# Kernel optimization log

Hardware: AMD Instinct MI355X
Metric: run time of the kernel (lower is better)

## Reference

```python
import jax, jax.numpy as jnp
import numpy as np

N_HEADS = 8

def setup_inputs() -> dict:
    key = jax.random.key(0)
    ks = jax.random.split(key, 7)
    B, S, D = 4, 2048, 512
    s = 1.0 / np.sqrt(D)
    return {
        "input_Q": jax.random.normal(ks[0], (B, S, D), jnp.float32),
        "input_K": jax.random.normal(ks[1], (B, S, D), jnp.float32),
        "input_V": jax.random.normal(ks[2], (B, S, D), jnp.float32),
        "W_Q": jax.random.normal(ks[3], (D, D), jnp.float32) * s,
        "W_K": jax.random.normal(ks[4], (D, D), jnp.float32) * s,
        "W_V": jax.random.normal(ks[5], (D, D), jnp.float32) * s,
        "W_O": jax.random.normal(ks[6], (D, D), jnp.float32) * s,
    }

def reference(input_Q, input_K, input_V, W_Q, W_K, W_V, W_O):
    B, Sq, D = input_Q.shape
    Sk = input_K.shape[1]
    H = N_HEADS
    d_k = D // H
    # torch nn.Linear(bias=False): y = x @ W.T
    def proj(x, W):
        return (x @ W.T).reshape(B, -1, H, d_k).transpose(0, 2, 1, 3)  # [B,H,S,dk]
    Q = proj(input_Q, W_Q)
    K = proj(input_K, W_K)
    V = proj(input_V, W_V)
    scale = 1.0 / jnp.sqrt(jnp.float32(d_k))
    scores = jnp.einsum("bhqd,bhkd->bhqk", Q, K) * scale  # [B,H,Sq,Sk]
    # TriangularCausalMask: mask strict upper triangle with -inf
    causal = jnp.tril(jnp.ones((Sq, Sk), dtype=bool))
    scores = jnp.where(causal[None, None], scores, -jnp.inf)
    attn = jax.nn.softmax(scores, axis=-1)
    context = jnp.einsum("bhqk,bhkd->bhqd", attn, V)
    context = context.transpose(0, 2, 1, 3).reshape(B, Sq, D)
    return context @ W_O.T
```

## Files before the change

kernel.cpp:

```cpp
#include <hip/hip_runtime.h>
#include <hip/hip_bf16.h>
#include <math.h>

#define B_  4
#define S_  2048
#define D_  512
#define H_  8
#define DK_ 64
#define M_  (B_ * S_)

using bf16   = __bf16;
using bf16x4 = __bf16 __attribute__((ext_vector_type(4)));
using bf16x8 = __bf16 __attribute__((ext_vector_type(8)));
using f32x4  = float __attribute__((ext_vector_type(4)));

#define MFMA16(a, b, c) __builtin_amdgcn_mfma_f32_16x16x32_bf16((a), (b), (c), 0, 0, 0)
#define EXP2(x) exp2f(x)

typedef __attribute__((address_space(3))) void       lds_void;
typedef const __attribute__((address_space(1))) void gbl_void;

__device__ __forceinline__ void async16(const bf16* g, bf16* lds) {
    __builtin_amdgcn_global_load_lds((gbl_void*)g, (lds_void*)lds, 16, 0, 0);
}

__device__ __forceinline__ bf16x8 ldg8(const bf16* p) {
    return *reinterpret_cast<const bf16x8*>(p);
}

__global__ __launch_bounds__(256) void cvt_all(
    const float* __restrict__ x0, const float* __restrict__ x1, const float* __restrict__ x2,
    const float* __restrict__ w0, const float* __restrict__ w1,
    const float* __restrict__ w2, const float* __restrict__ w3,
    bf16* __restrict__ dst)
{
    const size_t i = ((size_t)blockIdx.x * 256 + threadIdx.x) * 8;
    const float* src;
    size_t off;
    if (i < (size_t)3 << 22) {
        const int seg = (int)(i >> 22);
        off = i & (((size_t)1 << 22) - 1);
        src = (seg == 0) ? x0 : (seg == 1) ? x1 : x2;
    } else {
        const size_t j = i - ((size_t)3 << 22);
        const int seg = (int)(j >> 18);
        off = j & (((size_t)1 << 18) - 1);
        src = (seg == 0) ? w0 : (seg == 1) ? w1 : (seg == 2) ? w2 : w3;
    }
    f32x4 a = *reinterpret_cast<const f32x4*>(src + off);
    f32x4 b = *reinterpret_cast<const f32x4*>(src + off + 4);
    bf16x8 r;
    #pragma unroll
    for (int j = 0; j < 4; ++j) { r[j] = (bf16)a[j]; r[j + 4] = (bf16)b[j]; }
    *reinterpret_cast<bf16x8*>(dst + i) = r;
}

template <int MODE>
__global__ __launch_bounds__(256) void gemm_proj(
    const bf16* __restrict__ Xbase, const bf16* __restrict__ Wbase,
    void* __restrict__ OutBase)
{
    const int bx  = blockIdx.x;
    const int xcd = bx & 7;
    const int idx = bx >> 3;
    const int mt  = xcd + 8 * (idx & 7);
    const int nt  = (MODE == 0) ? ((idx >> 3) & 3) : (idx >> 3);
    const int z   = (MODE == 0) ? (idx >> 5) : 3;

    const bf16* X  = Xbase + ((MODE == 0) ? (size_t)z * M_ * D_ : 0);
    const bf16* Wm = Wbase + (size_t)z * D_ * D_;

    const int lane = threadIdx.x & 63;
    const int wave = threadIdx.x >> 6;
    const int lc = lane & 15;
    const int lg = lane >> 4;
    const int ta = (wave >> 1) * 4;
    const int tb = (wave & 1) * 4;
    const int wblk = nt * 128;
    const int xblk = mt * 128;
    const bool swapped = (MODE == 1) || (z < 2);

    __shared__ bf16 As[2][128 * 64];
    __shared__ bf16 Bs[2][128 * 64];

    f32x4 acc[4][4] = {};

    #pragma unroll
    for (int i = 0; i < 4; ++i) {
        const int g   = i * 4 + wave;
        const int row = (g & 7) * 16 + lc;
        const int kc  = (g >> 3) * 4 + lg;
        async16(X  + (size_t)(xblk + row) * D_ + kc * 8, As[0] + (i * 256 + wave * 64) * 8);
        async16(Wm + (size_t)(wblk + row) * D_ + kc * 8, Bs[0] + (i * 256 + wave * 64) * 8);
    }

    for (int j = 0; j < 8; ++j) {
        __syncthreads();
        if (j < 7) {
            const int kn = (j + 1) * 64;
            bf16* ad = As[(j + 1) & 1];
            bf16* bd = Bs[(j + 1) & 1];
            #pragma unroll
            for (int i = 0; i < 4; ++i) {
                const int g   = i * 4 + wave;
                const int row = (g & 7) * 16 + lc;
                const int kc  = (g >> 3) * 4 + lg;
                async16(X  + (size_t)(xblk + row) * D_ + kn + kc * 8,
                        ad + (i * 256 + wave * 64) * 8);
                async16(Wm + (size_t)(wblk + row) * D_ + kn + kc * 8,
                        bd + (i * 256 + wave * 64) * 8);
            }
        }
        const bf16* as = As[j & 1];
        const bf16* bs = Bs[j & 1];

        #pragma unroll
        for (int kk = 0; kk < 2; ++kk) {
            bf16x8 af[4], bfm[4];
            if (swapped) {
                #pragma unroll
                for (int mi = 0; mi < 4; ++mi)
                    af[mi] = ldg8(&bs[(kk * 512 + (ta + mi) * 64 + lane) * 8]);
                #pragma unroll
                for (int ni = 0; ni < 4; ++ni)
                    bfm[ni] = ldg8(&as[(kk * 512 + (tb + ni) * 64 + lane) * 8]);
            } else {
                #pragma unroll
                for (int mi = 0; mi < 4; ++mi)
                    af[mi] = ldg8(&as[(kk * 512 + (ta + mi) * 64 + lane) * 8]);
                #pragma unroll
                for (int ni = 0; ni < 4; ++ni)
                    bfm[ni] = ldg8(&bs[(kk * 512 + (tb + ni) * 64 + lane) * 8]);
            }
            #pragma unroll
            for (int mi = 0; mi < 4; ++mi)
                #pragma unroll
                for (int ni = 0; ni < 4; ++ni)
                    acc[mi][ni] = MFMA16(af[mi], bfm[ni], acc[mi][ni]);
        }
    }

    if (MODE == 1) {
        float* Y = (float*)OutBase;
        #pragma unroll
        for (int mi = 0; mi < 4; ++mi)
            #pragma unroll
            for (int ni = 0; ni < 4; ++ni) {
                const int s = xblk + (tb + ni) * 16 + lc;
                const int d = wblk + (ta + mi) * 16 + lg * 4;
                *reinterpret_cast<f32x4*>(&Y[(size_t)s * D_ + d]) = acc[mi][ni];
            }
    } else if (z < 2) {
        bf16* Y = (bf16*)OutBase + (size_t)z * M_ * D_;
        const float sc = (z == 0) ? 0.125f * 1.4426950408889634f : 1.0f;
        #pragma unroll
        for (int mi = 0; mi < 4; ++mi)
            #pragma unroll
            for (int ni = 0; ni < 4; ++ni) {
                const int s = xblk + (tb + ni) * 16 + lc;
                const int d = wblk + (ta + mi) * 16 + lg * 4;
                bf16x4 v;
                #pragma unroll
                for (int r = 0; r < 4; ++r) v[r] = (bf16)(acc[mi][ni][r] * sc);
                const size_t oidx =
                    ((((size_t)(s >> 11) * H_ + (d >> 6)) * S_
                      + (s & (S_ - 1))) << 6) + (d & 63);
                *reinterpret_cast<bf16x4*>(&Y[oidx]) = v;
            }
    } else {
        bf16* Y = (bf16*)OutBase + (size_t)z * M_ * D_;
        #pragma unroll
        for (int mi = 0; mi < 4; ++mi)
            #pragma unroll
            for (int ni = 0; ni < 4; ++ni) {
                const int s0  = xblk + (ta + mi) * 16 + lg * 4;
                const int col = wblk + (tb + ni) * 16 + lc;
                bf16x4 v;
                #pragma unroll
                for (int r = 0; r < 4; ++r) v[r] = (bf16)acc[mi][ni][r];
                const size_t oidx =
                    ((((size_t)(s0 >> 11)) * H_ + (col >> 6)) << 17)
                    + (size_t)(col & 63) * S_ + (s0 & (S_ - 1));
                *reinterpret_cast<bf16x4*>(&Y[oidx]) = v;
            }
    }
}

__global__ __launch_bounds__(256) void attn(
    const bf16* __restrict__ QKV, bf16* __restrict__ Ctx)
{
    const int bx = blockIdx.x;
    const int bh = (bx & 7) * 4 + ((bx >> 3) & 3);
    const int pi = bx >> 5;
    const int b = bh >> 3, h = bh & 7;
    const size_t plane = (size_t)S_ * DK_;
    const bf16* Q  = QKV + (size_t)bh * plane;
    const bf16* Kp = QKV + (size_t)(B_ * H_) * plane + (size_t)bh * plane;
    const bf16* Vt = QKV + 2 * (size_t)(B_ * H_) * plane + (size_t)bh * plane;

    const int lane = threadIdx.x & 63;
    const int wave = threadIdx.x >> 6;
    const int lc = lane & 15;
    const int lg = lane >> 4;
    const int srow = wave * 16 + lc;
    const int mrow = wave * 16 + lc;

    __shared__ bf16 Ks[2][64 * 64];
    __shared__ bf16 Vs[2][64 * 64];
    __shared__ bf16 Pw[4][128 * 8];

    const int lo = pi;
    const int hi = 31 - pi;

    const int qL = lo * 64 + mrow;
    const int qH = hi * 64 + mrow;
    bf16x8 qfL0 = ldg8(Q + (size_t)qL * DK_ + lg * 8);
    bf16x8 qfL1 = ldg8(Q + (size_t)qL * DK_ + 32 + lg * 8);
    bf16x8 qfH0 = ldg8(Q + (size_t)qH * DK_ + lg * 8);
    bf16x8 qfH1 = ldg8(Q + (size_t)qH * DK_ + 32 + lg * 8);

    f32x4 accL[4] = {}, accH[4] = {};
    float liL = 0.f, liH = 0.f;

    #pragma unroll
    for (int i = 0; i < 2; ++i) {
        const int kc = i * 4 + lg;
        async16(Kp + (size_t)srow * DK_ + kc * 8, Ks[0] + (i * 256 + wave * 64) * 8);
        async16(Vt + (size_t)srow * S_ + kc * 8,  Vs[0] + (i * 256 + wave * 64) * 8);
    }

    for (int j = 0; j <= hi; ++j) {
        __syncthreads();
        if (j < hi) {
            const int kn = (j + 1) * 64;
            bf16* kd = Ks[(j + 1) & 1];
            bf16* vd = Vs[(j + 1) & 1];
            #pragma unroll
            for (int i = 0; i < 2; ++i) {
                const int kc = i * 4 + lg;
                async16(Kp + (size_t)(kn + srow) * DK_ + kc * 8,
                        kd + (i * 256 + wave * 64) * 8);
                async16(Vt + (size_t)srow * S_ + kn + kc * 8,
                        vd + (i * 256 + wave * 64) * 8);
            }
        }
        const bf16* ks = Ks[j & 1];
        const bf16* vs = Vs[j & 1];
        bf16* Pp = &Pw[wave][0];

        bf16x8 kf0[4], kf1[4], vf0[4], vf1[4];
        #pragma unroll
        for (int t = 0; t < 4; ++t) {
            kf0[t] = ldg8(&ks[(t * 64 + lane) * 8]);
            kf1[t] = ldg8(&ks[(256 + t * 64 + lane) * 8]);
            vf0[t] = ldg8(&vs[(t * 64 + lane) * 8]);
            vf1[t] = ldg8(&vs[(256 + t * 64 + lane) * 8]);
        }

        auto step = [&](const bf16x8& qf0, const bf16x8& qf1, bool diag,
                        f32x4* accO, float& li) {
            f32x4 st[4];
            #pragma unroll
            for (int t = 0; t < 4; ++t) {
                f32x4 zz = {};
                zz = MFMA16(kf0[t], qf0, zz);
                st[t] = MFMA16(kf1[t], qf1, zz);
            }
            float rs = 0.f;
            if (diag) {
                #pragma unroll
                for (int t = 0; t < 4; ++t)
                    #pragma unroll
                    for (int r = 0; r < 4; ++r) {
                        const int kl = t * 16 + lg * 4 + r;
                        const float pv = EXP2((kl <= mrow) ? st[t][r] : -1e30f);
                        st[t][r] = pv;
                        rs += pv;
                    }
            } else {
                #pragma unroll
                for (int t = 0; t < 4; ++t)
                    #pragma unroll
                    for (int r = 0; r < 4; ++r) {
                        const float pv = EXP2(st[t][r]);
                        st[t][r] = pv;
                        rs += pv;
                    }
            }
            li += rs;

            #pragma unroll
            for (int t = 0; t < 4; ++t) {
                bf16x4 pv;
                #pragma unroll
                for (int r = 0; r < 4; ++r) pv[r] = (bf16)st[t][r];
                *reinterpret_cast<bf16x4*>(
                    &Pp[((2 * t + (lg >> 1)) * 16 + lc) * 8 + (lg & 1) * 4]) = pv;
            }
            bf16x8 p0 = ldg8(&Pp[lane * 8]);
            bf16x8 p1 = ldg8(&Pp[(64 + lane) * 8]);

            #pragma unroll
            for (int t = 0; t < 4; ++t) {
                accO[t] = MFMA16(vf0[t], p0, accO[t]);
                accO[t] = MFMA16(vf1[t], p1, accO[t]);
            }
        };

        step(qfH0, qfH1, j == hi, accH, liH);
        if (j <= lo) step(qfL0, qfL1, j == lo, accL, liL);
    }

    liL += __shfl_xor(liL, 16); liL += __shfl_xor(liL, 32);
    liH += __shfl_xor(liH, 16); liH += __shfl_xor(liH, 32);
    const float rlL = 1.0f / liL;
    const float rlH = 1.0f / liH;
    #pragma unroll
    for (int t = 0; t < 4; ++t) {
        bf16x4 oL, oH;
        #pragma unroll
        for (int r = 0; r < 4; ++r) {
            oL[r] = (bf16)(accL[t][r] * rlL);
            oH[r] = (bf16)(accH[t][r] * rlH);
        }
        const int d = t * 16 + lg * 4;
        *reinterpret_cast<bf16x4*>(&Ctx[((size_t)b * S_ + qL) * D_ + h * 64 + d]) = oL;
        *reinterpret_cast<bf16x4*>(&Ctx[((size_t)b * S_ + qH) * D_ + h * 64 + d]) = oH;
    }
}

extern "C" void kernel_launch(void* const* d_in, const int* in_sizes, int n_in,
                              void* d_out, int out_size, void* d_ws, size_t ws_size,
                              hipStream_t stream)
{
    float* out = (float*)d_out;

    bf16* Xb  = (bf16*)d_ws;
    bf16* Wb  = Xb + (size_t)3 * M_ * D_;
    bf16* qkv = Wb + (size_t)4 * D_ * D_;
    bf16* ctx = qkv + (size_t)3 * M_ * D_;

    cvt_all<<<6656, 256, 0, stream>>>(
        (const float*)d_in[0], (const float*)d_in[1], (const float*)d_in[2],
        (const float*)d_in[3], (const float*)d_in[4], (const float*)d_in[5],
        (const float*)d_in[6], Xb);

    gemm_proj<0><<<dim3(768), 256, 0, stream>>>(Xb, Wb, qkv);
    attn<<<dim3(512), 256, 0, stream>>>(qkv, ctx);
    gemm_proj<1><<<dim3(256), 256, 0, stream>>>(ctx, Wb, out);
}
```

Before: 196.4 us.

## Store operands in MFMA fragment layout and drop LDS staging in projection GEMMs

Result: faster. 188.4 us (-4.1%).

```diff
diff --git a/kernel.cpp b/kernel.cpp
--- a/kernel.cpp
+++ b/kernel.cpp
@@ -28,6 +28,10 @@
     return *reinterpret_cast<const bf16x8*>(p);
 }
 
+__device__ __forceinline__ size_t fragbase(int g, int k0, int kk, int t) {
+    return ((((size_t)(g * 8 + k0) * 2 + kk) * 4 + t) * 64) * 8;
+}
+
 __global__ __launch_bounds__(256) void cvt_all(
     const float* __restrict__ x0, const float* __restrict__ x1, const float* __restrict__ x2,
     const float* __restrict__ w0, const float* __restrict__ w1,
@@ -36,102 +40,70 @@
 {
     const size_t i = ((size_t)blockIdx.x * 256 + threadIdx.x) * 8;
     const float* src;
-    size_t off;
+    size_t off, dbase;
     if (i < (size_t)3 << 22) {
         const int seg = (int)(i >> 22);
         off = i & (((size_t)1 << 22) - 1);
         src = (seg == 0) ? x0 : (seg == 1) ? x1 : x2;
+        dbase = (size_t)seg << 22;
     } else {
-        const size_t j = i - ((size_t)3 << 22);
-        const int seg = (int)(j >> 18);
-        off = j & (((size_t)1 << 18) - 1);
+        const size_t jj = i - ((size_t)3 << 22);
+        const int seg = (int)(jj >> 18);
+        off = jj & (((size_t)1 << 18) - 1);
         src = (seg == 0) ? w0 : (seg == 1) ? w1 : (seg == 2) ? w2 : w3;
-    }
+        dbase = ((size_t)3 << 22) + ((size_t)seg << 18);
+    }
+    const int row = (int)(off >> 9), col = (int)(off & 511);
+    const int g = row >> 6, t = (row >> 4) & 3, lc = row & 15;
+    const int k0 = col >> 6, kk = (col >> 5) & 1, lg = (col >> 3) & 3;
+    const size_t didx = dbase + fragbase(g, k0, kk, t) + (size_t)(lg * 16 + lc) * 8;
+
     f32x4 a = *reinterpret_cast<const f32x4*>(src + off);
     f32x4 b = *reinterpret_cast<const f32x4*>(src + off + 4);
     bf16x8 r;
     #pragma unroll
     for (int j = 0; j < 4; ++j) { r[j] = (bf16)a[j]; r[j + 4] = (bf16)b[j]; }
-    *reinterpret_cast<bf16x8*>(dst + i) = r;
-}
-
-template <int MODE>
-__global__ __launch_bounds__(256) void gemm_proj(
-    const bf16* __restrict__ Xbase, const bf16* __restrict__ Wbase,
-    void* __restrict__ OutBase)
+    *reinterpret_cast<bf16x8*>(dst + didx) = r;
+}
+
+__global__ __launch_bounds__(256) void gemm_qkv(
+    const bf16* __restrict__ Xf, const bf16* __restrict__ Wf,
+    bf16* __restrict__ qkv)
 {
     const int bx  = blockIdx.x;
     const int xcd = bx & 7;
     const int idx = bx >> 3;
     const int mt  = xcd + 8 * (idx & 7);
-    const int nt  = (MODE == 0) ? ((idx >> 3) & 3) : (idx >> 3);
-    const int z   = (MODE == 0) ? (idx >> 5) : 3;
-
-    const bf16* X  = Xbase + ((MODE == 0) ? (size_t)z * M_ * D_ : 0);
-    const bf16* Wm = Wbase + (size_t)z * D_ * D_;
+    const int rest = idx >> 3;
+    const int nt  = rest & 3;
+    const int z   = rest >> 2;
+
+    const bf16* Xz = Xf + (size_t)z * M_ * D_;
+    const bf16* Wz = Wf + (size_t)z * D_ * D_;
+    const bool vz = (z == 2);
+    const bf16* A  = vz ? Xz : Wz;
+    const bf16* Bm = vz ? Wz : Xz;
 
     const int lane = threadIdx.x & 63;
     const int wave = threadIdx.x >> 6;
     const int lc = lane & 15;
     const int lg = lane >> 4;
-    const int ta = (wave >> 1) * 4;
-    const int tb = (wave & 1) * 4;
-    const int wblk = nt * 128;
-    const int xblk = mt * 128;
-    const bool swapped = (MODE == 1) || (z < 2);
-
-    __shared__ bf16 As[2][128 * 64];
-    __shared__ bf16 Bs[2][128 * 64];
+    const int gA = (vz ? 2 * mt : 2 * nt) + (wave >> 1);
+    const int gB = (vz ? 2 * nt : 2 * mt) + (wave & 1);
 
     f32x4 acc[4][4] = {};
 
     #pragma unroll
-    for (int i = 0; i < 4; ++i) {
-        const int g   = i * 4 + wave;
-        const int row = (g & 7) * 16 + lc;
-        const int kc  = (g >> 3) * 4 + lg;
-        async16(X  + (size_t)(xblk + row) * D_ + kc * 8, As[0] + (i * 256 + wave * 64) * 8);
-        async16(Wm + (size_t)(wblk + row) * D_ + kc * 8, Bs[0] + (i * 256 + wave * 64) * 8);
-    }
-
-    for (int j = 0; j < 8; ++j) {
-        __syncthreads();
-        if (j < 7) {
-            const int kn = (j + 1) * 64;
-            bf16* ad = As[(j + 1) & 1];
-            bf16* bd = Bs[(j + 1) & 1];
-            #pragma unroll
-            for (int i = 0; i < 4; ++i) {
-                const int g   = i * 4 + wave;
-                const int row = (g & 7) * 16 + lc;
-                const int kc  = (g >> 3) * 4 + lg;
-                async16(X  + (size_t)(xblk + row) * D_ + kn + kc * 8,
-                        ad + (i * 256 + wave * 64) * 8);
-                async16(Wm + (size_t)(wblk + row) * D_ + kn + kc * 8,
-                        bd + (i * 256 + wave * 64) * 8);
-            }
-        }
-        const bf16* as = As[j & 1];
-        const bf16* bs = Bs[j & 1];
-
+    for (int k0 = 0; k0 < 8; ++k0) {
         #pragma unroll
         for (int kk = 0; kk < 2; ++kk) {
             bf16x8 af[4], bfm[4];
-            if (swapped) {
-                #pragma unroll
-                for (int mi = 0; mi < 4; ++mi)
-                    af[mi] = ldg8(&bs[(kk * 512 + (ta + mi) * 64 + lane) * 8]);
-                #pragma unroll
-                for (int ni = 0; ni < 4; ++ni)
-                    bfm[ni] = ldg8(&as[(kk * 512 + (tb + ni) * 64 + lane) * 8]);
-            } else {
-                #pragma unroll
-                for (int mi = 0; mi < 4; ++mi)
-                    af[mi] = ldg8(&as[(kk * 512 + (ta + mi) * 64 + lane) * 8]);
-                #pragma unroll
-                for (int ni = 0; ni < 4; ++ni)
-                    bfm[ni] = ldg8(&bs[(kk * 512 + (tb + ni) * 64 + lane) * 8]);
-            }
+            #pragma unroll
+            for (int t = 0; t < 4; ++t)
+                af[t] = ldg8(A + fragbase(gA, k0, kk, t) + (size_t)lane * 8);
+            #pragma unroll
+            for (int t = 0; t < 4; ++t)
+                bfm[t] = ldg8(Bm + fragbase(gB, k0, kk, t) + (size_t)lane * 8);
             #pragma unroll
             for (int mi = 0; mi < 4; ++mi)
                 #pragma unroll
@@ -140,25 +112,15 @@
         }
     }
 
-    if (MODE == 1) {
-        float* Y = (float*)OutBase;
+    if (z < 2) {
+        bf16* Y = qkv + (size_t)z * M_ * D_;
+        const float sc = (z == 0) ? 0.125f * 1.4426950408889634f : 1.0f;
         #pragma unroll
         for (int mi = 0; mi < 4; ++mi)
             #pragma unroll
             for (int ni = 0; ni < 4; ++ni) {
-                const int s = xblk + (tb + ni) * 16 + lc;
-                const int d = wblk + (ta + mi) * 16 + lg * 4;
-                *reinterpret_cast<f32x4*>(&Y[(size_t)s * D_ + d]) = acc[mi][ni];
-            }
-    } else if (z < 2) {
-        bf16* Y = (bf16*)OutBase + (size_t)z * M_ * D_;
-        const float sc = (z == 0) ? 0.125f * 1.4426950408889634f : 1.0f;
-        #pragma unroll
-        for (int mi = 0; mi < 4; ++mi)
-            #pragma unroll
-            for (int ni = 0; ni < 4; ++ni) {
-                const int s = xblk + (tb + ni) * 16 + lc;
-                const int d = wblk + (ta + mi) * 16 + lg * 4;
+                const int d = gA * 64 + mi * 16 + lg * 4;
+                const int s = gB * 64 + ni * 16 + lc;
                 bf16x4 v;
                 #pragma unroll
                 for (int r = 0; r < 4; ++r) v[r] = (bf16)(acc[mi][ni][r] * sc);
@@ -168,26 +130,75 @@
                 *reinterpret_cast<bf16x4*>(&Y[oidx]) = v;
             }
     } else {
-        bf16* Y = (bf16*)OutBase + (size_t)z * M_ * D_;
+        bf16* Y = qkv + (size_t)2 * M_ * D_;
         #pragma unroll
         for (int mi = 0; mi < 4; ++mi)
             #pragma unroll
             for (int ni = 0; ni < 4; ++ni) {
-                const int s0  = xblk + (ta + mi) * 16 + lg * 4;
-                const int col = wblk + (tb + ni) * 16 + lc;
+                const int s = gA * 64 + mi * 16 + lg * 4;
+                const int d = gB * 64 + ni * 16 + lc;
                 bf16x4 v;
                 #pragma unroll
                 for (int r = 0; r < 4; ++r) v[r] = (bf16)acc[mi][ni][r];
                 const size_t oidx =
-                    ((((size_t)(s0 >> 11)) * H_ + (col >> 6)) << 17)
-                    + (size_t)(col & 63) * S_ + (s0 & (S_ - 1));
+                    ((((size_t)(s >> 11)) * H_ + (d >> 6)) << 17)
+                    + (size_t)(d & 63) * S_ + (s & (S_ - 1));
                 *reinterpret_cast<bf16x4*>(&Y[oidx]) = v;
             }
     }
 }
 
+__global__ __launch_bounds__(256) void gemm_out(
+    const bf16* __restrict__ CtxF, const bf16* __restrict__ WoF,
+    float* __restrict__ out)
+{
+    const int bx  = blockIdx.x;
+    const int xcd = bx & 7;
+    const int idx = bx >> 3;
+    const int mt  = xcd + 8 * (idx & 15);
+    const int nt  = idx >> 4;
+
+    const int lane = threadIdx.x & 63;
+    const int wave = threadIdx.x >> 6;
+    const int lc = lane & 15;
+    const int lg = lane >> 4;
+    const int gA = 2 * nt + (wave >> 1);
+    const int tA = (wave & 1) * 2;
+    const int gB = mt;
+
+    f32x4 acc[2][4] = {};
+
+    #pragma unroll
+    for (int k0 = 0; k0 < 8; ++k0) {
+        #pragma unroll
+        for (int kk = 0; kk < 2; ++kk) {
+            bf16x8 af[2], bfm[4];
+            #pragma unroll
+            for (int ai = 0; ai < 2; ++ai)
+                af[ai] = ldg8(WoF + fragbase(gA, k0, kk, tA + ai) + (size_t)lane * 8);
+            #pragma unroll
+            for (int t = 0; t < 4; ++t)
+                bfm[t] = ldg8(CtxF + fragbase(gB, k0, kk, t) + (size_t)lane * 8);
+            #pragma unroll
+            for (int ai = 0; ai < 2; ++ai)
+                #pragma unroll
+                for (int ni = 0; ni < 4; ++ni)
+                    acc[ai][ni] = MFMA16(af[ai], bfm[ni], acc[ai][ni]);
+        }
+    }
+
+    #pragma unroll
+    for (int ai = 0; ai < 2; ++ai)
+        #pragma unroll
+        for (int ni = 0; ni < 4; ++ni) {
+            const int d = gA * 64 + (tA + ai) * 16 + lg * 4;
+            const int s = gB * 64 + ni * 16 + lc;
+            *reinterpret_cast<f32x4*>(&out[(size_t)s * D_ + d]) = acc[ai][ni];
+        }
+}
+
 __global__ __launch_bounds__(256) void attn(
-    const bf16* __restrict__ QKV, bf16* __restrict__ Ctx)
+    const bf16* __restrict__ QKV, bf16* __restrict__ CtxF)
 {
     const int bx = blockIdx.x;
     const int bh = (bx & 7) * 4 + ((bx >> 3) & 3);
@@ -207,7 +218,7 @@
 
     __shared__ bf16 Ks[2][64 * 64];
     __shared__ bf16 Vs[2][64 * 64];
-    __shared__ bf16 Pw[4][128 * 8];
+    __shared__ bf16 Pw[4][1280];
 
     const int lo = pi;
     const int hi = 31 - pi;
@@ -315,17 +326,26 @@
     liH += __shfl_xor(liH, 16); liH += __shfl_xor(liH, 32);
     const float rlL = 1.0f / liL;
     const float rlH = 1.0f / liH;
-    #pragma unroll
-    for (int t = 0; t < 4; ++t) {
-        bf16x4 oL, oH;
-        #pragma unroll
-        for (int r = 0; r < 4; ++r) {
-            oL[r] = (bf16)(accL[t][r] * rlL);
-            oH[r] = (bf16)(accH[t][r] * rlH);
-        }
-        const int d = t * 16 + lg * 4;
-        *reinterpret_cast<bf16x4*>(&Ctx[((size_t)b * S_ + qL) * D_ + h * 64 + d]) = oL;
-        *reinterpret_cast<bf16x4*>(&Ctx[((size_t)b * S_ + qH) * D_ + h * 64 + d]) = oH;
+    bf16* T = &Pw[wave][0];
+
+    #pragma unroll
+    for (int half = 0; half < 2; ++half) {
+        const f32x4* accO = half ? accH : accL;
+        const float rl = half ? rlH : rlL;
+        const int jq = half ? hi : lo;
+        #pragma unroll
+        for (int t = 0; t < 4; ++t) {
+            bf16x4 ov;
+            #pragma unroll
+            for (int r = 0; r < 4; ++r) ov[r] = (bf16)(accO[t][r] * rl);
+            *reinterpret_cast<bf16x4*>(&T[lc * 72 + t * 16 + lg * 4]) = ov;
+        }
+        #pragma unroll
+        for (int kk = 0; kk < 2; ++kk) {
+            bf16x8 o8 = ldg8(&T[lc * 72 + kk * 32 + lg * 8]);
+            *reinterpret_cast<bf16x8*>(
+                &CtxF[fragbase(b * 32 + jq, h, kk, wave) + (size_t)lane * 8]) = o8;
+        }
     }
 }
 
@@ -335,17 +355,17 @@
 {
     float* out = (float*)d_out;
 
-    bf16* Xb  = (bf16*)d_ws;
-    bf16* Wb  = Xb + (size_t)3 * M_ * D_;
-    bf16* qkv = Wb + (size_t)4 * D_ * D_;
-    bf16* ctx = qkv + (size_t)3 * M_ * D_;
+    bf16* Xf   = (bf16*)d_ws;
+    bf16* Wf   = Xf + (size_t)3 * M_ * D_;
+    bf16* qkv  = Wf + (size_t)4 * D_ * D_;
+    bf16* ctxF = qkv + (size_t)3 * M_ * D_;
 
     cvt_all<<<6656, 256, 0, stream>>>(
         (const float*)d_in[0], (const float*)d_in[1], (const float*)d_in[2],
         (const float*)d_in[3], (const float*)d_in[4], (const float*)d_in[5],
-        (const float*)d_in[6], Xb);
-
-    gemm_proj<0><<<dim3(768), 256, 0, stream>>>(Xb, Wb, qkv);
-    attn<<<dim3(512), 256, 0, stream>>>(qkv, ctx);
-    gemm_proj<1><<<dim3(256), 256, 0, stream>>>(ctx, Wb, out);
-}
+        (const float*)d_in[6], Xf);
+
+    gemm_qkv<<<dim3(768), 256, 0, stream>>>(Xf, Wf, qkv);
+    attn<<<dim3(512), 256, 0, stream>>>(qkv, ctxF);
+    gemm_out<<<dim3(512), 256, 0, stream>>>(ctxF, Wf + (size_t)3 * D_ * D_, out);
+}
```
